# Optimization experiments

Hardware: AMD Instinct MI355X
Metric: run time of the kernel (lower is better)

Reference implementation:

```python
import jax, jax.numpy as jnp
import numpy as np

B, N = 64, 4096

def setup_inputs() -> dict:
    key = jax.random.key(0)
    k1, k2, k3, k4, k5, k6 = jax.random.split(key, 6)
    return {
        "V_mag": jax.random.uniform(k1, (B, N), dtype=jnp.float32, minval=0.9, maxval=1.1),
        "V_ang": 0.3 * jax.random.normal(k2, (B, N), dtype=jnp.float32),
        "P_in": jax.random.normal(k3, (B, N), dtype=jnp.float32),
        "Q_in": jax.random.normal(k4, (B, N), dtype=jnp.float32),
        "G_bus": jax.random.normal(k5, (N, N), dtype=jnp.float32) / np.sqrt(N),
        "B_bus": jax.random.normal(k6, (N, N), dtype=jnp.float32) / np.sqrt(N),
    }

def reference(V_mag, V_ang, P_in, Q_in, G_bus, B_bus):
    # P_i = V_i sum_j V_j (G_ij cos(ti-tj) + B_ij sin(ti-tj))
    # Q_i = V_i sum_j V_j (G_ij sin(ti-tj) - B_ij cos(ti-tj))
    # Angle-addition rewrite (exact): with c_j = V_j cos(t_j), s_j = V_j sin(t_j):
    #   sum_j G_ij V_j cos(ti-tj) = cos(ti)*(G c)_i + sin(ti)*(G s)_i, etc.
    cos_t = jnp.cos(V_ang)  # [B, N]
    sin_t = jnp.sin(V_ang)
    c = V_mag * cos_t       # V_j cos(t_j)
    s = V_mag * sin_t       # V_j sin(t_j)
    Gc = jnp.einsum('ij,bj->bi', G_bus, c)
    Gs = jnp.einsum('ij,bj->bi', G_bus, s)
    Bc = jnp.einsum('ij,bj->bi', B_bus, c)
    Bs = jnp.einsum('ij,bj->bi', B_bus, s)
    # sum_j V_j (G cos + B sin) = cos_ti*(Gc+Bs) + sin_ti*(Gs-Bc)
    P_calc = V_mag * (cos_t * (Gc + Bs) + sin_t * (Gs - Bc))
    # sum_j V_j (G sin - B cos) = sin_ti*(Gc+Bs) - cos_ti*(Gs-Bc)
    Q_calc = V_mag * (sin_t * (Gc + Bs) - cos_t * (Gs - Bc))
    res_P = P_calc - P_in
    res_Q = Q_calc - Q_in
    return (res_P, res_Q)
```

## Files before the change

### kernel.cpp

```cpp
#include <hip/hip_runtime.h>
#include <stdint.h>

#define N_DIM 4096
#define B_DIM 64
#define OUTSZ (B_DIM * N_DIM)

typedef __bf16 bf16x8 __attribute__((ext_vector_type(8)));
typedef float floatx4 __attribute__((ext_vector_type(4)));

union FragU { uint4 u; bf16x8 h; };

__device__ __forceinline__ unsigned short f2bf_rne(float f) {
    unsigned int u = __float_as_uint(f);
    u += 0x7fffu + ((u >> 16) & 1u);
    return (unsigned short)(u >> 16);
}

__global__ __launch_bounds__(256) void pf_prep(
        const float* __restrict__ Vmag, const float* __restrict__ Vang,
        unsigned short* __restrict__ c_pk, unsigned short* __restrict__ s_pk,
        float* __restrict__ c_f, float* __restrict__ s_f) {
    int idx = blockIdx.x * 256 + threadIdx.x;
    int b = idx >> 12;
    int j = idx & 4095;
    float sv, cv;
    sincosf(Vang[idx], &sv, &cv);
    float v = Vmag[idx];
    float c = v * cv;
    float s = v * sv;
    c_f[idx] = c;
    s_f[idx] = s;
    int p = (((j >> 3) << 6) + b) * 8 + (j & 7);
    c_pk[p] = f2bf_rne(c);
    s_pk[p] = f2bf_rne(s);
}

__global__ __launch_bounds__(1024, 4) void pf_gemm(
        const float* __restrict__ G, const float* __restrict__ Bm,
        const unsigned short* __restrict__ c_pk, const unsigned short* __restrict__ s_pk,
        float* __restrict__ ws_part) {
    __shared__ float redX[3][4][16][66];
    __shared__ float redY[3][4][16][66];
    const int tid = threadIdx.x;
    const int wave = tid >> 6;
    const int lane = tid & 63;
    const int n = lane & 15;
    const int quad = lane >> 4;
    const int kc = blockIdx.x & 3;
    const int rg = blockIdx.x >> 2;
    const int stripe = wave & 3;
    const int kq = wave >> 2;

    const int row = (rg << 6) + (stripe << 4) + n;
    const int kb = (kc << 10) + (kq << 8);

    const float* gp = G  + (size_t)row * N_DIM + kb + (quad << 3);
    const float* bp = Bm + (size_t)row * N_DIM + kb + (quad << 3);
    const unsigned short* cp = c_pk + ((size_t)((kb >> 3) + quad) * 64 + n) * 8;
    const unsigned short* sp = s_pk + ((size_t)((kb >> 3) + quad) * 64 + n) * 8;

    floatx4 accX[4], accY[4];
    #pragma unroll
    for (int t = 0; t < 4; ++t) {
        accX[t] = (floatx4){0.f, 0.f, 0.f, 0.f};
        accY[t] = (floatx4){0.f, 0.f, 0.f, 0.f};
    }

    float4 g0 = *(const float4*)gp;
    float4 g1 = *(const float4*)(gp + 4);
    float4 h0 = *(const float4*)bp;
    float4 h1 = *(const float4*)(bp + 4);
    gp += 32; bp += 32;

    #pragma unroll 1
    for (int it = 0; it < 8; ++it) {
        uint4 cu[4], su[4];
        #pragma unroll
        for (int t = 0; t < 4; ++t) cu[t] = *(const uint4*)(cp + t * 128);
        #pragma unroll
        for (int t = 0; t < 4; ++t) su[t] = *(const uint4*)(sp + t * 128);
        cp += 2048; sp += 2048;

        float4 ng0, ng1, nh0, nh1;
        if (it < 7) {
            ng0 = *(const float4*)gp;
            ng1 = *(const float4*)(gp + 4);
            nh0 = *(const float4*)bp;
            nh1 = *(const float4*)(bp + 4);
            gp += 32; bp += 32;
        }

        bf16x8 ag, ah;
        ag[0] = (__bf16)g0.x; ag[1] = (__bf16)g0.y; ag[2] = (__bf16)g0.z; ag[3] = (__bf16)g0.w;
        ag[4] = (__bf16)g1.x; ag[5] = (__bf16)g1.y; ag[6] = (__bf16)g1.z; ag[7] = (__bf16)g1.w;
        ah[0] = (__bf16)h0.x; ah[1] = (__bf16)h0.y; ah[2] = (__bf16)h0.z; ah[3] = (__bf16)h0.w;
        ah[4] = (__bf16)h1.x; ah[5] = (__bf16)h1.y; ah[6] = (__bf16)h1.z; ah[7] = (__bf16)h1.w;

        #pragma unroll
        for (int t = 0; t < 4; ++t) {
            FragU cf, nf;
            cf.u = cu[t];
            nf.u.x = cu[t].x ^ 0x80008000u;
            nf.u.y = cu[t].y ^ 0x80008000u;
            nf.u.z = cu[t].z ^ 0x80008000u;
            nf.u.w = cu[t].w ^ 0x80008000u;
            accX[t] = __builtin_amdgcn_mfma_f32_16x16x32_bf16(ag, cf.h, accX[t], 0, 0, 0);
            accY[t] = __builtin_amdgcn_mfma_f32_16x16x32_bf16(ah, nf.h, accY[t], 0, 0, 0);
        }
        #pragma unroll
        for (int t = 0; t < 4; ++t) {
            FragU sf;
            sf.u = su[t];
            accX[t] = __builtin_amdgcn_mfma_f32_16x16x32_bf16(ah, sf.h, accX[t], 0, 0, 0);
            accY[t] = __builtin_amdgcn_mfma_f32_16x16x32_bf16(ag, sf.h, accY[t], 0, 0, 0);
        }

        if (it < 7) { g0 = ng0; g1 = ng1; h0 = nh0; h1 = nh1; }
    }

    if (kq > 0) {
        #pragma unroll
        for (int t = 0; t < 4; ++t)
            #pragma unroll
            for (int r = 0; r < 4; ++r) {
                redX[kq - 1][stripe][(quad << 2) + r][(t << 4) + n] = accX[t][r];
                redY[kq - 1][stripe][(quad << 2) + r][(t << 4) + n] = accY[t][r];
            }
    }
    __syncthreads();
    if (kq == 0) {
        #pragma unroll
        for (int t = 0; t < 4; ++t)
            #pragma unroll
            for (int r = 0; r < 4; ++r) {
                float x = accX[t][r], y = accY[t][r];
                #pragma unroll
                for (int w = 0; w < 3; ++w) {
                    x += redX[w][stripe][(quad << 2) + r][(t << 4) + n];
                    y += redY[w][stripe][(quad << 2) + r][(t << 4) + n];
                }
                accX[t][r] = x; accY[t][r] = y;
            }
        float* wsX = ws_part + (size_t)kc * OUTSZ;
        float* wsY = ws_part + (size_t)(4 + kc) * OUTSZ;
        const int rowbase = (rg << 6) + (stripe << 4) + (quad << 2);
        #pragma unroll
        for (int t = 0; t < 4; ++t) {
            size_t off = (size_t)((t << 4) + n) * N_DIM + rowbase;
            *(float4*)(wsX + off) = (float4){accX[t][0], accX[t][1], accX[t][2], accX[t][3]};
            *(float4*)(wsY + off) = (float4){accY[t][0], accY[t][1], accY[t][2], accY[t][3]};
        }
    }
}

__global__ __launch_bounds__(256) void pf_reduce(
        const float* __restrict__ ws_part,
        const float* __restrict__ c_f, const float* __restrict__ s_f,
        const float* __restrict__ P_in, const float* __restrict__ Q_in,
        float* __restrict__ out) {
    int e = (blockIdx.x * 256 + threadIdx.x) * 4;
    float4 X = *(const float4*)(ws_part + e);
    float4 Y = *(const float4*)(ws_part + 4 * OUTSZ + e);
    #pragma unroll
    for (int kc = 1; kc < 4; ++kc) {
        float4 x = *(const float4*)(ws_part + (size_t)kc * OUTSZ + e);
        float4 y = *(const float4*)(ws_part + (size_t)(4 + kc) * OUTSZ + e);
        X.x += x.x; X.y += x.y; X.z += x.z; X.w += x.w;
        Y.x += y.x; Y.y += y.y; Y.z += y.z; Y.w += y.w;
    }
    float4 c = *(const float4*)(c_f + e);
    float4 s = *(const float4*)(s_f + e);
    float4 P = *(const float4*)(P_in + e);
    float4 Q = *(const float4*)(Q_in + e);
    float4 rp, rq;
    rp.x = c.x * X.x + s.x * Y.x - P.x;  rq.x = s.x * X.x - c.x * Y.x - Q.x;
    rp.y = c.y * X.y + s.y * Y.y - P.y;  rq.y = s.y * X.y - c.y * Y.y - Q.y;
    rp.z = c.z * X.z + s.z * Y.z - P.z;  rq.z = s.z * X.z - c.z * Y.z - Q.z;
    rp.w = c.w * X.w + s.w * Y.w - P.w;  rq.w = s.w * X.w - c.w * Y.w - Q.w;
    *(float4*)(out + e) = rp;
    *(float4*)(out + OUTSZ + e) = rq;
}

extern "C" void kernel_launch(void* const* d_in, const int* in_sizes, int n_in,
                              void* d_out, int out_size, void* d_ws, size_t ws_size,
                              hipStream_t stream) {
    const float* Vmag = (const float*)d_in[0];
    const float* Vang = (const float*)d_in[1];
    const float* P_in = (const float*)d_in[2];
    const float* Q_in = (const float*)d_in[3];
    const float* G    = (const float*)d_in[4];
    const float* Bm   = (const float*)d_in[5];
    float* out = (float*)d_out;

    char* ws = (char*)d_ws;
    unsigned short* c_pk = (unsigned short*)(ws);
    unsigned short* s_pk = (unsigned short*)(ws + (512u << 10));
    float* c_f = (float*)(ws + (1u << 20));
    float* s_f = (float*)(ws + (2u << 20));
    float* ws_part = (float*)(ws + (3u << 20));

    hipLaunchKernelGGL(pf_prep, dim3((B_DIM * N_DIM) / 256), dim3(256), 0, stream,
                       Vmag, Vang, c_pk, s_pk, c_f, s_f);
    hipLaunchKernelGGL(pf_gemm, dim3(256), dim3(1024), 0, stream,
                       G, Bm, c_pk, s_pk, ws_part);
    hipLaunchKernelGGL(pf_reduce, dim3(OUTSZ / 1024), dim3(256), 0, stream,
                       ws_part, c_f, s_f, P_in, Q_in, out);
}
```

Measured before the change: 182.1 us.

## Stage packed c/s operands through LDS with double-buffered global_load_lds

The c/s bf16 operand tiles are now loaded cooperatively into double-buffered shared memory with direct global-to-LDS loads, so the four row-stripe waves share them instead of each re-reading from global memory. The K interleaving across waves changes so that each 256-wide k-phase is split among the four q groups, and the reduction scratch reuses the same LDS buffer. This is meant to cut redundant global/L2 traffic for the B operand. In exchange it adds a block barrier per phase and a larger LDS footprint, which may limit occupancy.

```diff
diff --git a/kernel.cpp b/kernel.cpp
--- a/kernel.cpp
+++ b/kernel.cpp
@@ -9,6 +9,13 @@
 typedef float floatx4 __attribute__((ext_vector_type(4)));
 
 union FragU { uint4 u; bf16x8 h; };
+
+#define AS1 __attribute__((address_space(1)))
+#define AS3 __attribute__((address_space(3)))
+
+__device__ __forceinline__ void gll16(const void* gp, void* lp) {
+    __builtin_amdgcn_global_load_lds((const AS1 void*)gp, (AS3 void*)lp, 16, 0, 0);
+}
 
 __device__ __forceinline__ unsigned short f2bf_rne(float f) {
     unsigned int u = __float_as_uint(f);
@@ -39,8 +46,7 @@
         const float* __restrict__ G, const float* __restrict__ Bm,
         const unsigned short* __restrict__ c_pk, const unsigned short* __restrict__ s_pk,
         float* __restrict__ ws_part) {
-    __shared__ float redX[3][4][16][66];
-    __shared__ float redY[3][4][16][66];
+    __shared__ __align__(16) unsigned short cs[2][2][16384];
     const int tid = threadIdx.x;
     const int wave = tid >> 6;
     const int lane = tid & 63;
@@ -49,15 +55,27 @@
     const int kc = blockIdx.x & 3;
     const int rg = blockIdx.x >> 2;
     const int stripe = wave & 3;
-    const int kq = wave >> 2;
+    const int q = wave >> 2;
 
     const int row = (rg << 6) + (stripe << 4) + n;
-    const int kb = (kc << 10) + (kq << 8);
-
-    const float* gp = G  + (size_t)row * N_DIM + kb + (quad << 3);
-    const float* bp = Bm + (size_t)row * N_DIM + kb + (quad << 3);
-    const unsigned short* cp = c_pk + ((size_t)((kb >> 3) + quad) * 64 + n) * 8;
-    const unsigned short* sp = s_pk + ((size_t)((kb >> 3) + quad) * 64 + n) * 8;
+    const int kbase = kc << 10;
+
+    const float* gp0 = G  + (size_t)row * N_DIM + kbase + (q << 6) + (quad << 3);
+    const float* bp0 = Bm + (size_t)row * N_DIM + kbase + (q << 6) + (quad << 3);
+
+    const int sj = wave << 1;
+    const unsigned short* csrc = c_pk + (kc << 16) + (sj << 9) + (lane << 3);
+    const unsigned short* ssrc = s_pk + (kc << 16) + (sj << 9) + (lane << 3);
+
+    auto stage = [&](int p) {
+        const int bp = p & 1;
+        const unsigned short* c0 = csrc + (p << 14);
+        const unsigned short* s0 = ssrc + (p << 14);
+        gll16(c0,       &cs[bp][0][sj << 9]);
+        gll16(c0 + 512, &cs[bp][0][(sj + 1) << 9]);
+        gll16(s0,       &cs[bp][1][sj << 9]);
+        gll16(s0 + 512, &cs[bp][1][(sj + 1) << 9]);
+    };
 
     floatx4 accX[4], accY[4];
     #pragma unroll
@@ -66,69 +84,83 @@
         accY[t] = (floatx4){0.f, 0.f, 0.f, 0.f};
     }
 
-    float4 g0 = *(const float4*)gp;
-    float4 g1 = *(const float4*)(gp + 4);
-    float4 h0 = *(const float4*)bp;
-    float4 h1 = *(const float4*)(bp + 4);
-    gp += 32; bp += 32;
-
-    #pragma unroll 1
-    for (int it = 0; it < 8; ++it) {
-        uint4 cu[4], su[4];
-        #pragma unroll
-        for (int t = 0; t < 4; ++t) cu[t] = *(const uint4*)(cp + t * 128);
-        #pragma unroll
-        for (int t = 0; t < 4; ++t) su[t] = *(const uint4*)(sp + t * 128);
-        cp += 2048; sp += 2048;
-
-        float4 ng0, ng1, nh0, nh1;
-        if (it < 7) {
-            ng0 = *(const float4*)gp;
-            ng1 = *(const float4*)(gp + 4);
-            nh0 = *(const float4*)bp;
-            nh1 = *(const float4*)(bp + 4);
-            gp += 32; bp += 32;
+    stage(0);
+    float4 g0 = *(const float4*)gp0;
+    float4 g1 = *(const float4*)(gp0 + 4);
+    float4 h0 = *(const float4*)bp0;
+    float4 h1 = *(const float4*)(bp0 + 4);
+
+    #pragma unroll
+    for (int p = 0; p < 4; ++p) {
+        __syncthreads();
+        if (p < 3) stage(p + 1);
+        const int bp = p & 1;
+
+        #pragma unroll
+        for (int i = 0; i < 2; ++i) {
+            const int pi = (p << 1) + i;
+            float4 ng0, ng1, nh0, nh1;
+            if (pi < 7) {
+                const int noff = (((pi + 1) >> 1) << 8) + (((pi + 1) & 1) << 5);
+                const float* gn = gp0 + noff;
+                const float* bn = bp0 + noff;
+                ng0 = *(const float4*)gn; ng1 = *(const float4*)(gn + 4);
+                nh0 = *(const float4*)bn; nh1 = *(const float4*)(bn + 4);
+            }
+
+            const int kl = (((q << 1) + i) << 2) + quad;
+            const unsigned short* cl = &cs[bp][0][(kl << 9) + (n << 3)];
+            const unsigned short* sl = &cs[bp][1][(kl << 9) + (n << 3)];
+            uint4 cu[4], su[4];
+            #pragma unroll
+            for (int t = 0; t < 4; ++t) cu[t] = *(const uint4*)(cl + (t << 7));
+            #pragma unroll
+            for (int t = 0; t < 4; ++t) su[t] = *(const uint4*)(sl + (t << 7));
+
+            bf16x8 ag, ah;
+            ag[0] = (__bf16)g0.x; ag[1] = (__bf16)g0.y; ag[2] = (__bf16)g0.z; ag[3] = (__bf16)g0.w;
+            ag[4] = (__bf16)g1.x; ag[5] = (__bf16)g1.y; ag[6] = (__bf16)g1.z; ag[7] = (__bf16)g1.w;
+            ah[0] = (__bf16)h0.x; ah[1] = (__bf16)h0.y; ah[2] = (__bf16)h0.z; ah[3] = (__bf16)h0.w;
+            ah[4] = (__bf16)h1.x; ah[5] = (__bf16)h1.y; ah[6] = (__bf16)h1.z; ah[7] = (__bf16)h1.w;
+
+            #pragma unroll
+            for (int t = 0; t < 4; ++t) {
+                FragU cf, nf;
+                cf.u = cu[t];
+                nf.u.x = cu[t].x ^ 0x80008000u;
+                nf.u.y = cu[t].y ^ 0x80008000u;
+                nf.u.z = cu[t].z ^ 0x80008000u;
+                nf.u.w = cu[t].w ^ 0x80008000u;
+                accX[t] = __builtin_amdgcn_mfma_f32_16x16x32_bf16(ag, cf.h, accX[t], 0, 0, 0);
+                accY[t] = __builtin_amdgcn_mfma_f32_16x16x32_bf16(ah, nf.h, accY[t], 0, 0, 0);
+            }
+            #pragma unroll
+            for (int t = 0; t < 4; ++t) {
+                FragU sf;
+                sf.u = su[t];
+                accX[t] = __builtin_amdgcn_mfma_f32_16x16x32_bf16(ah, sf.h, accX[t], 0, 0, 0);
+                accY[t] = __builtin_amdgcn_mfma_f32_16x16x32_bf16(ag, sf.h, accY[t], 0, 0, 0);
+            }
+
+            if (pi < 7) { g0 = ng0; g1 = ng1; h0 = nh0; h1 = nh1; }
         }
-
-        bf16x8 ag, ah;
-        ag[0] = (__bf16)g0.x; ag[1] = (__bf16)g0.y; ag[2] = (__bf16)g0.z; ag[3] = (__bf16)g0.w;
-        ag[4] = (__bf16)g1.x; ag[5] = (__bf16)g1.y; ag[6] = (__bf16)g1.z; ag[7] = (__bf16)g1.w;
-        ah[0] = (__bf16)h0.x; ah[1] = (__bf16)h0.y; ah[2] = (__bf16)h0.z; ah[3] = (__bf16)h0.w;
-        ah[4] = (__bf16)h1.x; ah[5] = (__bf16)h1.y; ah[6] = (__bf16)h1.z; ah[7] = (__bf16)h1.w;
-
-        #pragma unroll
-        for (int t = 0; t < 4; ++t) {
-            FragU cf, nf;
-            cf.u = cu[t];
-            nf.u.x = cu[t].x ^ 0x80008000u;
-            nf.u.y = cu[t].y ^ 0x80008000u;
-            nf.u.z = cu[t].z ^ 0x80008000u;
-            nf.u.w = cu[t].w ^ 0x80008000u;
-            accX[t] = __builtin_amdgcn_mfma_f32_16x16x32_bf16(ag, cf.h, accX[t], 0, 0, 0);
-            accY[t] = __builtin_amdgcn_mfma_f32_16x16x32_bf16(ah, nf.h, accY[t], 0, 0, 0);
-        }
-        #pragma unroll
-        for (int t = 0; t < 4; ++t) {
-            FragU sf;
-            sf.u = su[t];
-            accX[t] = __builtin_amdgcn_mfma_f32_16x16x32_bf16(ah, sf.h, accX[t], 0, 0, 0);
-            accY[t] = __builtin_amdgcn_mfma_f32_16x16x32_bf16(ag, sf.h, accY[t], 0, 0, 0);
-        }
-
-        if (it < 7) { g0 = ng0; g1 = ng1; h0 = nh0; h1 = nh1; }
-    }
-
-    if (kq > 0) {
+    }
+
+    float* red = (float*)&cs[0][0][0];
+    #define RX(k, s_, m, b) red[((((k) * 4 + (s_)) * 16 + (m)) * 66) + (b)]
+    #define RY(k, s_, m, b) red[12672 + ((((k) * 4 + (s_)) * 16 + (m)) * 66) + (b)]
+    __syncthreads();
+    if (q > 0) {
         #pragma unroll
         for (int t = 0; t < 4; ++t)
             #pragma unroll
             for (int r = 0; r < 4; ++r) {
-                redX[kq - 1][stripe][(quad << 2) + r][(t << 4) + n] = accX[t][r];
-                redY[kq - 1][stripe][(quad << 2) + r][(t << 4) + n] = accY[t][r];
+                RX(q - 1, stripe, (quad << 2) + r, (t << 4) + n) = accX[t][r];
+                RY(q - 1, stripe, (quad << 2) + r, (t << 4) + n) = accY[t][r];
             }
     }
     __syncthreads();
-    if (kq == 0) {
+    if (q == 0) {
         #pragma unroll
         for (int t = 0; t < 4; ++t)
             #pragma unroll
@@ -136,8 +168,8 @@
                 float x = accX[t][r], y = accY[t][r];
                 #pragma unroll
                 for (int w = 0; w < 3; ++w) {
-                    x += redX[w][stripe][(quad << 2) + r][(t << 4) + n];
-                    y += redY[w][stripe][(quad << 2) + r][(t << 4) + n];
+                    x += RX(w, stripe, (quad << 2) + r, (t << 4) + n);
+                    y += RY(w, stripe, (quad << 2) + r, (t << 4) + n);
                 }
                 accX[t][r] = x; accY[t][r] = y;
             }
```

Measured after the change: 170.6 us. 6.3% less time.

## Stage c/s fragments in LDS and retile GEMM to 128 rows by 8 K-splits

Applied to the files above, without the earlier changes.

Each block now copies its 512-wide K slice of the packed bf16 c/s vectors into LDS once, and all 16 waves read their MFMA B-fragments from LDS instead of global memory. The tiling changes from 64 rows by a 4-way K split to 128 rows by an 8-way K split, with two waves per stripe reduced through LDS. This cuts redundant global and L2 traffic for c/s. In exchange the split-K workspace doubles to 8 partials and the reduce kernel reads twice as much, and the 128KB LDS buffer limits blocks per CU.

```diff
diff --git a/kernel.cpp b/kernel.cpp
--- a/kernel.cpp
+++ b/kernel.cpp
@@ -39,25 +39,32 @@
         const float* __restrict__ G, const float* __restrict__ Bm,
         const unsigned short* __restrict__ c_pk, const unsigned short* __restrict__ s_pk,
         float* __restrict__ ws_part) {
-    __shared__ float redX[3][4][16][66];
-    __shared__ float redY[3][4][16][66];
+    __shared__ __align__(16) unsigned short lds_cs[65536];
     const int tid = threadIdx.x;
     const int wave = tid >> 6;
     const int lane = tid & 63;
     const int n = lane & 15;
     const int quad = lane >> 4;
-    const int kc = blockIdx.x & 3;
-    const int rg = blockIdx.x >> 2;
-    const int stripe = wave & 3;
-    const int kq = wave >> 2;
-
-    const int row = (rg << 6) + (stripe << 4) + n;
-    const int kb = (kc << 10) + (kq << 8);
-
+    const int rg = blockIdx.x >> 3;
+    const int kc = blockIdx.x & 7;
+    const int stripe = wave & 7;
+    const int t2 = wave >> 3;
+
+    {
+        const unsigned short* csrc = c_pk + ((size_t)kc << 15);
+        const unsigned short* ssrc = s_pk + ((size_t)kc << 15);
+        #pragma unroll
+        for (int j = 0; j < 4; ++j) {
+            const int o = (j << 13) + (tid << 3);
+            *(uint4*)&lds_cs[o]         = *(const uint4*)(csrc + o);
+            *(uint4*)&lds_cs[32768 + o] = *(const uint4*)(ssrc + o);
+        }
+    }
+
+    const int row = (rg << 7) + (stripe << 4) + n;
+    const int kb = (kc << 9) + (t2 << 8);
     const float* gp = G  + (size_t)row * N_DIM + kb + (quad << 3);
     const float* bp = Bm + (size_t)row * N_DIM + kb + (quad << 3);
-    const unsigned short* cp = c_pk + ((size_t)((kb >> 3) + quad) * 64 + n) * 8;
-    const unsigned short* sp = s_pk + ((size_t)((kb >> 3) + quad) * 64 + n) * 8;
 
     floatx4 accX[4], accY[4];
     #pragma unroll
@@ -72,15 +79,10 @@
     float4 h1 = *(const float4*)(bp + 4);
     gp += 32; bp += 32;
 
+    __syncthreads();
+
     #pragma unroll 1
     for (int it = 0; it < 8; ++it) {
-        uint4 cu[4], su[4];
-        #pragma unroll
-        for (int t = 0; t < 4; ++t) cu[t] = *(const uint4*)(cp + t * 128);
-        #pragma unroll
-        for (int t = 0; t < 4; ++t) su[t] = *(const uint4*)(sp + t * 128);
-        cp += 2048; sp += 2048;
-
         float4 ng0, ng1, nh0, nh1;
         if (it < 7) {
             ng0 = *(const float4*)gp;
@@ -89,6 +91,14 @@
             nh1 = *(const float4*)(bp + 4);
             gp += 32; bp += 32;
         }
+
+        const int kg = (t2 << 5) + (it << 2) + quad;
+        const int fo = (kg << 9) + (n << 3);
+        uint4 cu[4], su[4];
+        #pragma unroll
+        for (int t = 0; t < 4; ++t) cu[t] = *(const uint4*)&lds_cs[fo + (t << 7)];
+        #pragma unroll
+        for (int t = 0; t < 4; ++t) su[t] = *(const uint4*)&lds_cs[32768 + fo + (t << 7)];
 
         bf16x8 ag, ah;
         ag[0] = (__bf16)g0.x; ag[1] = (__bf16)g0.y; ag[2] = (__bf16)g0.z; ag[3] = (__bf16)g0.w;
@@ -118,37 +128,34 @@
         if (it < 7) { g0 = ng0; g1 = ng1; h0 = nh0; h1 = nh1; }
     }
 
-    if (kq > 0) {
+    float* red = (float*)lds_cs;
+    #define RD(x, s_, m, bb) red[((((x) * 8 + (s_)) * 16 + (m)) * 66) + (bb)]
+    __syncthreads();
+    if (t2 == 1) {
         #pragma unroll
         for (int t = 0; t < 4; ++t)
             #pragma unroll
             for (int r = 0; r < 4; ++r) {
-                redX[kq - 1][stripe][(quad << 2) + r][(t << 4) + n] = accX[t][r];
-                redY[kq - 1][stripe][(quad << 2) + r][(t << 4) + n] = accY[t][r];
+                RD(0, stripe, (quad << 2) + r, (t << 4) + n) = accX[t][r];
+                RD(1, stripe, (quad << 2) + r, (t << 4) + n) = accY[t][r];
             }
     }
     __syncthreads();
-    if (kq == 0) {
-        #pragma unroll
-        for (int t = 0; t < 4; ++t)
+    if (t2 == 0) {
+        float* wsX = ws_part + (size_t)kc * OUTSZ;
+        float* wsY = ws_part + (size_t)(8 + kc) * OUTSZ;
+        const int rowbase = (rg << 7) + (stripe << 4) + (quad << 2);
+        #pragma unroll
+        for (int t = 0; t < 4; ++t) {
+            float4 X, Y;
             #pragma unroll
             for (int r = 0; r < 4; ++r) {
-                float x = accX[t][r], y = accY[t][r];
-                #pragma unroll
-                for (int w = 0; w < 3; ++w) {
-                    x += redX[w][stripe][(quad << 2) + r][(t << 4) + n];
-                    y += redY[w][stripe][(quad << 2) + r][(t << 4) + n];
-                }
-                accX[t][r] = x; accY[t][r] = y;
+                ((float*)&X)[r] = accX[t][r] + RD(0, stripe, (quad << 2) + r, (t << 4) + n);
+                ((float*)&Y)[r] = accY[t][r] + RD(1, stripe, (quad << 2) + r, (t << 4) + n);
             }
-        float* wsX = ws_part + (size_t)kc * OUTSZ;
-        float* wsY = ws_part + (size_t)(4 + kc) * OUTSZ;
-        const int rowbase = (rg << 6) + (stripe << 4) + (quad << 2);
-        #pragma unroll
-        for (int t = 0; t < 4; ++t) {
             size_t off = (size_t)((t << 4) + n) * N_DIM + rowbase;
-            *(float4*)(wsX + off) = (float4){accX[t][0], accX[t][1], accX[t][2], accX[t][3]};
-            *(float4*)(wsY + off) = (float4){accY[t][0], accY[t][1], accY[t][2], accY[t][3]};
+            *(float4*)(wsX + off) = X;
+            *(float4*)(wsY + off) = Y;
         }
     }
 }
@@ -160,11 +167,11 @@
         float* __restrict__ out) {
     int e = (blockIdx.x * 256 + threadIdx.x) * 4;
     float4 X = *(const float4*)(ws_part + e);
-    float4 Y = *(const float4*)(ws_part + 4 * OUTSZ + e);
+    float4 Y = *(const float4*)(ws_part + 8 * OUTSZ + e);
     #pragma unroll
-    for (int kc = 1; kc < 4; ++kc) {
+    for (int kc = 1; kc < 8; ++kc) {
         float4 x = *(const float4*)(ws_part + (size_t)kc * OUTSZ + e);
-        float4 y = *(const float4*)(ws_part + (size_t)(4 + kc) * OUTSZ + e);
+        float4 y = *(const float4*)(ws_part + (size_t)(8 + kc) * OUTSZ + e);
         X.x += x.x; X.y += x.y; X.z += x.z; X.w += x.w;
         Y.x += y.x; Y.y += y.y; Y.z += y.z; Y.w += y.w;
     }
```

Result: faster. 174.6 us (-4.1%).
